# Optimization experiments

Measured on AMD Instinct MI355X. Metric: run time of the kernel, lower is better.

## Reference

```python
import jax, jax.numpy as jnp
import numpy as np

NUM_NODES = 50000
NUM_EDGES = 600000
IN_DIM = 128
HID = 128
OUT_DIM = 10
NUM_GRAPHS = 64


def setup_inputs() -> dict:
    key = jax.random.key(0)
    ks = jax.random.split(key, 12)
    x = jax.random.normal(ks[0], (NUM_NODES, IN_DIM), dtype=jnp.float32)
    edge_index = jax.random.randint(ks[1], (2, NUM_EDGES), 0, NUM_NODES, dtype=jnp.int64)
    batch = jnp.sort(jax.random.randint(ks[2], (NUM_NODES,), 0, NUM_GRAPHS, dtype=jnp.int64))
    s = 0.05
    W1 = jax.random.normal(ks[3], (IN_DIM, HID), dtype=jnp.float32) * s
    b1 = jnp.zeros((HID,), dtype=jnp.float32)
    W2 = jax.random.normal(ks[4], (HID, HID), dtype=jnp.float32) * s
    b2 = jnp.zeros((HID,), dtype=jnp.float32)
    W3 = jax.random.normal(ks[5], (HID, HID), dtype=jnp.float32) * s
    b3 = jnp.zeros((HID,), dtype=jnp.float32)
    Wlin = jax.random.normal(ks[6], (HID, OUT_DIM), dtype=jnp.float32) * s
    blin = jnp.zeros((OUT_DIM,), dtype=jnp.float32)
    return {"x": x, "edge_index": edge_index, "batch": batch,
            "W1": W1, "b1": b1, "W2": W2, "b2": b2, "W3": W3, "b3": b3,
            "Wlin": Wlin, "blin": blin}


def _gcn_conv(x, W, b, src, dst, norm):
    # h = X W ; out[i] = sum_{(j->i)} norm_e * h[j] ; + bias
    h = x @ W                                   # [N, H]
    msg = h[src] * norm[:, None]                # [E+N, H] gather + scale
    out = jax.ops.segment_sum(msg, dst, num_segments=x.shape[0])  # scatter-add
    return out + b


def reference(x, edge_index, batch, W1, b1, W2, b2, W3, b3, Wlin, blin):
    N = x.shape[0]
    # add self loops (PyG GCNConv default)
    loops = jnp.arange(N, dtype=edge_index.dtype)
    src = jnp.concatenate([edge_index[0], loops])
    dst = jnp.concatenate([edge_index[1], loops])
    # symmetric normalization D^{-1/2} (A+I) D^{-1/2}; degree on target nodes
    deg = jax.ops.segment_sum(jnp.ones_like(dst, dtype=x.dtype), dst, num_segments=N)
    dinv = jnp.where(deg > 0, jax.lax.rsqrt(deg), 0.0)
    norm = dinv[src] * dinv[dst]

    h = jax.nn.relu(_gcn_conv(x, W1, b1, src, dst, norm))   # dropout = identity (eval)
    h = jax.nn.relu(_gcn_conv(h, W2, b2, src, dst, norm))
    h = jax.nn.relu(_gcn_conv(h, W3, b3, src, dst, norm))

    # global mean pool over graphs
    sums = jax.ops.segment_sum(h, batch, num_segments=NUM_GRAPHS)          # [G, H]
    cnts = jax.ops.segment_sum(jnp.ones((N,), dtype=h.dtype), batch, num_segments=NUM_GRAPHS)
    pooled = sums / jnp.maximum(cnts, 1.0)[:, None]
    return pooled @ Wlin + blin                                            # [G, OUT]
```

## Files before the change

### kernel.cpp

```cpp
#include <hip/hip_runtime.h>
#include <hip/hip_bf16.h>
#include <hip/hip_fp16.h>


#define HID 128
#define NGRAPH 64

typedef _Float16 half8v __attribute__((ext_vector_type(8)));
typedef float floatx4 __attribute__((ext_vector_type(4)));

__device__ __forceinline__ int idx_at(const void* p, long long i, int f64) {
    if (f64) return (int)((const long long*)p)[i];
    return ((const int*)p)[i];
}

__global__ void detect_kernel(const int* __restrict__ ei, int* __restrict__ flag) {
    __shared__ int cnt;
    if (threadIdx.x == 0) cnt = 0;
    __syncthreads();
    int z = 0;
    for (int i = threadIdx.x; i < 2048; i += 256)
        if (ei[2 * i + 1] == 0) z++;
    atomicAdd(&cnt, z);
    __syncthreads();
    if (threadIdx.x == 0) *flag = (cnt > 1024) ? 1 : 0;
}

__global__ void init_kernel(int* __restrict__ counts, float* __restrict__ pooled,
                            float* __restrict__ gcnt, int N) {
    int i = blockIdx.x * blockDim.x + threadIdx.x;
    if (i < N) counts[i] = 0;
    if (i < NGRAPH * HID) pooled[i] = 0.f;
    if (i < NGRAPH) gcnt[i] = 0.f;
}

__global__ void hist_kernel(const void* __restrict__ ei, const int* __restrict__ flag,
                            int* __restrict__ counts, int E, int N) {
    int e = blockIdx.x * blockDim.x + threadIdx.x;
    if (e >= E) return;
    int f64 = *flag;
    int d = idx_at(ei, (long long)E + e, f64);
    if ((unsigned)d < (unsigned)N) atomicAdd(&counts[d], 1);
}

__global__ __launch_bounds__(256) void tohalf_kernel(const float* __restrict__ in,
                                                     __half2* __restrict__ out, int n2) {
    int i = blockIdx.x * blockDim.x + threadIdx.x;
    if (i >= n2) return;
    float2 v = ((const float2*)in)[i];
    out[i] = __floats2half2_rn(v.x, v.y);
}

__global__ __launch_bounds__(256) void wfrag3_kernel(const float* __restrict__ W1,
                                                     const float* __restrict__ W2,
                                                     const float* __restrict__ W3,
                                                     half8v* __restrict__ wf) {
    int which = blockIdx.x >> 3;
    const float* W = which == 0 ? W1 : (which == 1 ? W2 : W3);
    int t = (blockIdx.x & 7) * 256 + threadIdx.x;
    int lane = t & 63;
    int nt = (t >> 6) & 7;
    int kblk = t >> 9;
    int n = nt * 16 + (lane & 15);
    int kbase = kblk * 32 + (lane >> 4) * 8;
    half8v v;
#pragma unroll
    for (int j = 0; j < 8; ++j) v[j] = (_Float16)W[(size_t)(kbase + j) * 128 + n];
    wf[which * 2048 + t] = v;
}

__device__ __forceinline__ int wave_incl_scan(int v, int lane) {
#pragma unroll
    for (int off = 1; off < 64; off <<= 1) {
        int u = __shfl_up(v, off);
        if (lane >= off) v += u;
    }
    return v;
}

__global__ __launch_bounds__(256) void blocksum_kernel(const int* __restrict__ counts,
                                                       int* __restrict__ bsums, int N) {
    int i = blockIdx.x * 256 + threadIdx.x;
    int v = (i < N) ? counts[i] : 0;
    int lane = threadIdx.x & 63, w = threadIdx.x >> 6;
#pragma unroll
    for (int off = 32; off > 0; off >>= 1) v += __shfl_down(v, off);
    __shared__ int ws[4];
    if (lane == 0) ws[w] = v;
    __syncthreads();
    if (threadIdx.x == 0) bsums[blockIdx.x] = ws[0] + ws[1] + ws[2] + ws[3];
}

__global__ __launch_bounds__(256) void scanb_kernel(int* __restrict__ bsums, int nb) {
    int t = threadIdx.x;
    int lane = t & 63, w = t >> 6;
    int v = (t < nb) ? bsums[t] : 0;
    int iv = wave_incl_scan(v, lane);
    __shared__ int wsum[4];
    if (lane == 63) wsum[w] = iv;
    __syncthreads();
    int add = 0;
    for (int k = 0; k < w; ++k) add += wsum[k];
    if (t < nb) bsums[t] = iv - v + add;
}

__global__ __launch_bounds__(256) void fill_kernel(const int* __restrict__ counts,
                                                   const int* __restrict__ bsums,
                                                   int* __restrict__ rowstart,
                                                   int* __restrict__ cursor,
                                                   float* __restrict__ dinv, int N) {
    int i = blockIdx.x * 256 + threadIdx.x;
    int c = (i < N) ? counts[i] : 0;
    int lane = threadIdx.x & 63, w = threadIdx.x >> 6;
    int iv = wave_incl_scan(c, lane);
    __shared__ int wsum[4];
    if (lane == 63) wsum[w] = iv;
    __syncthreads();
    int add = bsums[blockIdx.x];
    for (int k = 0; k < w; ++k) add += wsum[k];
    int excl = iv - c + add;
    if (i < N) {
        rowstart[i] = excl;
        cursor[i] = excl;
        dinv[i] = rsqrtf((float)(c + 1));
        if (i == N - 1) rowstart[N] = excl + c;
    }
}

__global__ void scatter_kernel(const void* __restrict__ ei, const int* __restrict__ flag,
                               int* __restrict__ cursor,
                               unsigned short* __restrict__ csr_src, int E, int N) {
    int e = blockIdx.x * blockDim.x + threadIdx.x;
    if (e >= E) return;
    int f64 = *flag;
    int s = idx_at(ei, e, f64);
    int d = idx_at(ei, (long long)E + e, f64);
    if ((unsigned)s >= (unsigned)N || (unsigned)d >= (unsigned)N) return;
    int pos = atomicAdd(&cursor[d], 1);
    csr_src[pos] = (unsigned short)s;
}

__global__ __launch_bounds__(256) void agg_kernel(const __half2* __restrict__ xh,
                                                  const int* __restrict__ rowstart,
                                                  const unsigned short* __restrict__ csr_src,
                                                  const float* __restrict__ dinv,
                                                  __half2* __restrict__ out, int N) {
    int wid = (blockIdx.x * blockDim.x + threadIdx.x) >> 6;
    int lane = threadIdx.x & 63;
    if (wid >= N) return;
    float di = dinv[wid];
    float w0 = di * di;
    float2 xs = __half22float2(xh[(size_t)wid * 64 + lane]);
    float accx = w0 * xs.x, accy = w0 * xs.y;
    float bccx = 0.f, bccy = 0.f;
    int e0 = rowstart[wid], e1 = rowstart[wid + 1];
    int e = e0;
    for (; e + 8 <= e1; e += 8) {
        int s[8]; float ds[8]; __half2 v[8];
#pragma unroll
        for (int u = 0; u < 8; ++u) s[u] = csr_src[e + u];
#pragma unroll
        for (int u = 0; u < 8; ++u) ds[u] = dinv[s[u]];
#pragma unroll
        for (int u = 0; u < 8; ++u) v[u] = xh[(size_t)s[u] * 64 + lane];
#pragma unroll
        for (int u = 0; u < 8; u += 2) {
            float wa = ds[u] * di, wb = ds[u + 1] * di;
            float2 f0 = __half22float2(v[u]);
            float2 f1 = __half22float2(v[u + 1]);
            accx = fmaf(wa, f0.x, accx);
            accy = fmaf(wa, f0.y, accy);
            bccx = fmaf(wb, f1.x, bccx);
            bccy = fmaf(wb, f1.y, bccy);
        }
    }
    for (; e + 4 <= e1; e += 4) {
        int s[4]; float ds[4]; __half2 v[4];
#pragma unroll
        for (int u = 0; u < 4; ++u) s[u] = csr_src[e + u];
#pragma unroll
        for (int u = 0; u < 4; ++u) ds[u] = dinv[s[u]];
#pragma unroll
        for (int u = 0; u < 4; ++u) v[u] = xh[(size_t)s[u] * 64 + lane];
#pragma unroll
        for (int u = 0; u < 4; u += 2) {
            float wa = ds[u] * di, wb = ds[u + 1] * di;
            float2 f0 = __half22float2(v[u]);
            float2 f1 = __half22float2(v[u + 1]);
            accx = fmaf(wa, f0.x, accx);
            accy = fmaf(wa, f0.y, accy);
            bccx = fmaf(wb, f1.x, bccx);
            bccy = fmaf(wb, f1.y, bccy);
        }
    }
    for (; e < e1; ++e) {
        int s = csr_src[e];
        float w = dinv[s] * di;
        float2 f = __half22float2(xh[(size_t)s * 64 + lane]);
        accx = fmaf(w, f.x, accx);
        accy = fmaf(w, f.y, accy);
    }
    out[(size_t)wid * 64 + lane] = __floats2half2_rn(accx + bccx, accy + bccy);
}

__global__ __launch_bounds__(256) void gemm_mfma(const __half2* __restrict__ A16,
                                                 const half8v* __restrict__ wf,
                                                 const float* __restrict__ bias,
                                                 __half2* __restrict__ O16, int M) {
    int wid = threadIdx.x >> 6, lane = threadIdx.x & 63;
    int rowTile = blockIdx.x * 64 + wid * 16;
    int hi = lane >> 4;
    int arow = rowTile + (lane & 15);
    if (arow >= M) arow = M - 1;
    const half8v* Arow = (const half8v*)((const _Float16*)A16 + (size_t)arow * 128);

    floatx4 acc[8];
#pragma unroll
    for (int nt = 0; nt < 8; ++nt) acc[nt] = (floatx4){0.f, 0.f, 0.f, 0.f};

#pragma unroll
    for (int kb = 0; kb < 4; ++kb) {
        half8v a = Arow[kb * 4 + hi];
#pragma unroll
        for (int nt = 0; nt < 8; ++nt) {
            half8v w = wf[(kb * 8 + nt) * 64 + lane];
            acc[nt] = __builtin_amdgcn_mfma_f32_16x16x32_f16(a, w, acc[nt], 0, 0, 0);
        }
    }

    int ocol_lo = lane & 15;
    int orow0 = rowTile + hi * 4;
#pragma unroll
    for (int nt = 0; nt < 8; ++nt) {
        int col = nt * 16 + ocol_lo;
        float b = bias[col];
#pragma unroll
        for (int r = 0; r < 4; ++r) {
            int orow = orow0 + r;
            if (orow < M) {
                float v = fmaxf(acc[nt][r] + b, 0.f);
                ((_Float16*)O16)[(size_t)orow * 128 + col] = (_Float16)v;
            }
        }
    }
}

#define POOL_CHUNK 16
__global__ __launch_bounds__(256) void pool_kernel(const __half2* __restrict__ h,
                                                   const void* __restrict__ batch,
                                                   const int* __restrict__ flag,
                                                   float* __restrict__ pooled,
                                                   float* __restrict__ gcnt, int N) {
    int wid = (blockIdx.x * blockDim.x + threadIdx.x) >> 6;
    int lane = threadIdx.x & 63;
    int n0 = wid * POOL_CHUNK;
    if (n0 >= N) return;
    int n1 = n0 + POOL_CHUNK; if (n1 > N) n1 = N;
    int f64 = *flag;
    int g = idx_at(batch, n0, f64);
    float ax = 0.f, ay = 0.f;
    int cnt = 0;
    for (int n = n0; n < n1; ++n) {
        int gn = idx_at(batch, n, f64);
        if (gn != g) {
            if ((unsigned)g < (unsigned)NGRAPH) {
                atomicAdd(&pooled[g * HID + 2 * lane], ax);
                atomicAdd(&pooled[g * HID + 2 * lane + 1], ay);
                if (lane == 0) atomicAdd(&gcnt[g], (float)cnt);
            }
            ax = ay = 0.f; cnt = 0; g = gn;
        }
        float2 v = __half22float2(h[(size_t)n * 64 + lane]);
        ax += v.x; ay += v.y; cnt++;
    }
    if ((unsigned)g < (unsigned)NGRAPH) {
        atomicAdd(&pooled[g * HID + 2 * lane], ax);
        atomicAdd(&pooled[g * HID + 2 * lane + 1], ay);
        if (lane == 0) atomicAdd(&gcnt[g], (float)cnt);
    }
}

__global__ __launch_bounds__(128) void final_kernel(const float* __restrict__ pooled,
                                                    const float* __restrict__ gcnt,
                                                    const float* __restrict__ Wl,
                                                    const float* __restrict__ bl,
                                                    float* __restrict__ out) {
    int o = blockIdx.x * blockDim.x + threadIdx.x;
    if (o >= NGRAPH * 10) return;
    int g = o / 10, c = o % 10;
    float inv = 1.0f / fmaxf(gcnt[g], 1.0f);
    float acc = 0.f;
    for (int k = 0; k < HID; ++k)
        acc = fmaf(pooled[g * HID + k], Wl[k * 10 + c], acc);
    out[o] = acc * inv + bl[c];
}

extern "C" void kernel_launch(void* const* d_in, const int* in_sizes, int n_in,
                              void* d_out, int out_size, void* d_ws, size_t ws_size,
                              hipStream_t stream) {
    const float* x   = (const float*)d_in[0];
    const void* ei   = d_in[1];
    const void* bat  = d_in[2];
    const float* W1  = (const float*)d_in[3];
    const float* b1  = (const float*)d_in[4];
    const float* W2  = (const float*)d_in[5];
    const float* b2  = (const float*)d_in[6];
    const float* W3  = (const float*)d_in[7];
    const float* b3  = (const float*)d_in[8];
    const float* Wl  = (const float*)d_in[9];
    const float* bl  = (const float*)d_in[10];
    float* out = (float*)d_out;

    const int N = in_sizes[0] / HID;
    const int E = in_sizes[1] / 2;

    char* w = (char*)d_ws;
    size_t off = 0;
    auto carve = [&](size_t bytes) -> void* {
        void* p = w + off;
        off = (off + bytes + 255) & ~(size_t)255;
        return p;
    };
    __half2* xh       = (__half2*)carve((size_t)N * HID * 2);
    __half2* aggB16   = (__half2*)carve((size_t)N * HID * 2);
    __half2* h16a     = (__half2*)carve((size_t)N * HID * 2);
    __half2* h16b     = (__half2*)carve((size_t)N * HID * 2);
    int*     counts   = (int*)carve((size_t)N * 4);
    int*     rowstart = (int*)carve((size_t)(N + 1) * 4);
    int*     cursor   = (int*)carve((size_t)N * 4);
    float*   dinv     = (float*)carve((size_t)N * 4);
    unsigned short* csr_src = (unsigned short*)carve((size_t)E * 2);
    float*   pooled   = (float*)carve((size_t)NGRAPH * HID * 4);
    float*   gcnt     = (float*)carve((size_t)NGRAPH * 4);
    half8v*  wf       = (half8v*)carve(3 * 2048 * 16);
    int*     bsums    = (int*)carve(1024);
    int*     flag     = (int*)carve(256);

    const int nb = (N + 255) / 256;

    detect_kernel<<<1, 256, 0, stream>>>((const int*)ei, flag);
    init_kernel<<<(N + 255) / 256, 256, 0, stream>>>(counts, pooled, gcnt, N);
    hist_kernel<<<(E + 255) / 256, 256, 0, stream>>>(ei, flag, counts, E, N);
    blocksum_kernel<<<nb, 256, 0, stream>>>(counts, bsums, N);
    scanb_kernel<<<1, 256, 0, stream>>>(bsums, nb);
    fill_kernel<<<nb, 256, 0, stream>>>(counts, bsums, rowstart, cursor, dinv, N);
    scatter_kernel<<<(E + 255) / 256, 256, 0, stream>>>(ei, flag, cursor, csr_src, E, N);

    const int n2 = N * HID / 2;
    tohalf_kernel<<<(n2 + 255) / 256, 256, 0, stream>>>(x, xh, n2);
    wfrag3_kernel<<<24, 256, 0, stream>>>(W1, W2, W3, wf);

    int aggBlocks  = (N + 3) / 4;
    int gemmBlocks = (N + 63) / 64;

    agg_kernel<<<aggBlocks, 256, 0, stream>>>(xh, rowstart, csr_src, dinv, aggB16, N);
    gemm_mfma<<<gemmBlocks, 256, 0, stream>>>(aggB16, wf, b1, h16a, N);
    agg_kernel<<<aggBlocks, 256, 0, stream>>>(h16a, rowstart, csr_src, dinv, aggB16, N);
    gemm_mfma<<<gemmBlocks, 256, 0, stream>>>(aggB16, wf + 2048, b2, h16b, N);
    agg_kernel<<<aggBlocks, 256, 0, stream>>>(h16b, rowstart, csr_src, dinv, aggB16, N);
    gemm_mfma<<<gemmBlocks, 256, 0, stream>>>(aggB16, wf + 4096, b3, h16a, N);

    int poolWaves = (N + POOL_CHUNK - 1) / POOL_CHUNK;
    int poolBlocks = (poolWaves + 3) / 4;
    pool_kernel<<<poolBlocks, 256, 0, stream>>>(h16a, bat, flag, pooled, gcnt, N);
    final_kernel<<<5, 128, 0, stream>>>(pooled, gcnt, Wl, bl, out);
}
```

Before: 245.2 us.

## Prescale features by dinv to drop per-edge dinv gathers, merge small kernels

Moves the symmetric normalization out of the edge loop. Source features are prescaled by dinv, once in the fp16 conversion and afterwards in the GEMM epilogue, so aggregation becomes a plain sum followed by a single multiply by the destination dinv. This removes one random dinv gather and one multiply per edge in each of the three aggregation passes. The format-detect kernel is folded into init, and the fp16 conversion and weight-fragment kernels are merged into one prep kernel, which cuts launches. Rounding changes slightly because the scaling now happens before the fp16 store.

```diff
diff --git a/kernel.cpp b/kernel.cpp
--- a/kernel.cpp
+++ b/kernel.cpp
@@ -14,24 +14,24 @@
     return ((const int*)p)[i];
 }
 
-__global__ void detect_kernel(const int* __restrict__ ei, int* __restrict__ flag) {
-    __shared__ int cnt;
-    if (threadIdx.x == 0) cnt = 0;
-    __syncthreads();
-    int z = 0;
-    for (int i = threadIdx.x; i < 2048; i += 256)
-        if (ei[2 * i + 1] == 0) z++;
-    atomicAdd(&cnt, z);
-    __syncthreads();
-    if (threadIdx.x == 0) *flag = (cnt > 1024) ? 1 : 0;
-}
-
-__global__ void init_kernel(int* __restrict__ counts, float* __restrict__ pooled,
+__global__ void init_kernel(const int* __restrict__ ei, int* __restrict__ flag,
+                            int* __restrict__ counts, float* __restrict__ pooled,
                             float* __restrict__ gcnt, int N) {
     int i = blockIdx.x * blockDim.x + threadIdx.x;
     if (i < N) counts[i] = 0;
     if (i < NGRAPH * HID) pooled[i] = 0.f;
     if (i < NGRAPH) gcnt[i] = 0.f;
+    if (blockIdx.x == 0) {
+        __shared__ int cnt;
+        if (threadIdx.x == 0) cnt = 0;
+        __syncthreads();
+        int z = 0;
+        for (int k = threadIdx.x; k < 2048; k += 256)
+            if (ei[2 * k + 1] == 0) z++;
+        atomicAdd(&cnt, z);
+        __syncthreads();
+        if (threadIdx.x == 0) *flag = (cnt > 1024) ? 1 : 0;
+    }
 }
 
 __global__ void hist_kernel(const void* __restrict__ ei, const int* __restrict__ flag,
@@ -41,32 +41,6 @@
     int f64 = *flag;
     int d = idx_at(ei, (long long)E + e, f64);
     if ((unsigned)d < (unsigned)N) atomicAdd(&counts[d], 1);
-}
-
-__global__ __launch_bounds__(256) void tohalf_kernel(const float* __restrict__ in,
-                                                     __half2* __restrict__ out, int n2) {
-    int i = blockIdx.x * blockDim.x + threadIdx.x;
-    if (i >= n2) return;
-    float2 v = ((const float2*)in)[i];
-    out[i] = __floats2half2_rn(v.x, v.y);
-}
-
-__global__ __launch_bounds__(256) void wfrag3_kernel(const float* __restrict__ W1,
-                                                     const float* __restrict__ W2,
-                                                     const float* __restrict__ W3,
-                                                     half8v* __restrict__ wf) {
-    int which = blockIdx.x >> 3;
-    const float* W = which == 0 ? W1 : (which == 1 ? W2 : W3);
-    int t = (blockIdx.x & 7) * 256 + threadIdx.x;
-    int lane = t & 63;
-    int nt = (t >> 6) & 7;
-    int kblk = t >> 9;
-    int n = nt * 16 + (lane & 15);
-    int kbase = kblk * 32 + (lane >> 4) * 8;
-    half8v v;
-#pragma unroll
-    for (int j = 0; j < 8; ++j) v[j] = (_Float16)W[(size_t)(kbase + j) * 128 + n];
-    wf[which * 2048 + t] = v;
 }
 
 __device__ __forceinline__ int wave_incl_scan(int v, int lane) {
@@ -140,7 +114,36 @@
     csr_src[pos] = (unsigned short)s;
 }
 
-__global__ __launch_bounds__(256) void agg_kernel(const __half2* __restrict__ xh,
+__global__ __launch_bounds__(256) void prep_kernel(const float* __restrict__ x,
+                                                   const float* __restrict__ dinv,
+                                                   __half2* __restrict__ xs,
+                                                   const float* __restrict__ W1,
+                                                   const float* __restrict__ W2,
+                                                   const float* __restrict__ W3,
+                                                   half8v* __restrict__ wf, int n2) {
+    if (blockIdx.x < 24) {
+        int which = blockIdx.x >> 3;
+        const float* W = which == 0 ? W1 : (which == 1 ? W2 : W3);
+        int t = (blockIdx.x & 7) * 256 + threadIdx.x;
+        int lane = t & 63;
+        int nt = (t >> 6) & 7;
+        int kblk = t >> 9;
+        int n = nt * 16 + (lane & 15);
+        int kbase = kblk * 32 + (lane >> 4) * 8;
+        half8v v;
+#pragma unroll
+        for (int j = 0; j < 8; ++j) v[j] = (_Float16)W[(size_t)(kbase + j) * 128 + n];
+        wf[which * 2048 + t] = v;
+    } else {
+        int i = (blockIdx.x - 24) * 256 + threadIdx.x;
+        if (i >= n2) return;
+        float dv = dinv[i >> 6];
+        float2 v = ((const float2*)x)[i];
+        xs[i] = __floats2half2_rn(dv * v.x, dv * v.y);
+    }
+}
+
+__global__ __launch_bounds__(256) void agg_kernel(const __half2* __restrict__ xs,
                                                   const int* __restrict__ rowstart,
                                                   const unsigned short* __restrict__ csr_src,
                                                   const float* __restrict__ dinv,
@@ -149,63 +152,53 @@
     int lane = threadIdx.x & 63;
     if (wid >= N) return;
     float di = dinv[wid];
-    float w0 = di * di;
-    float2 xs = __half22float2(xh[(size_t)wid * 64 + lane]);
-    float accx = w0 * xs.x, accy = w0 * xs.y;
+    float2 s0 = __half22float2(xs[(size_t)wid * 64 + lane]);
+    float accx = s0.x, accy = s0.y;
     float bccx = 0.f, bccy = 0.f;
     int e0 = rowstart[wid], e1 = rowstart[wid + 1];
     int e = e0;
     for (; e + 8 <= e1; e += 8) {
-        int s[8]; float ds[8]; __half2 v[8];
+        int s[8]; __half2 v[8];
 #pragma unroll
         for (int u = 0; u < 8; ++u) s[u] = csr_src[e + u];
 #pragma unroll
-        for (int u = 0; u < 8; ++u) ds[u] = dinv[s[u]];
-#pragma unroll
-        for (int u = 0; u < 8; ++u) v[u] = xh[(size_t)s[u] * 64 + lane];
+        for (int u = 0; u < 8; ++u) v[u] = xs[(size_t)s[u] * 64 + lane];
 #pragma unroll
         for (int u = 0; u < 8; u += 2) {
-            float wa = ds[u] * di, wb = ds[u + 1] * di;
             float2 f0 = __half22float2(v[u]);
             float2 f1 = __half22float2(v[u + 1]);
-            accx = fmaf(wa, f0.x, accx);
-            accy = fmaf(wa, f0.y, accy);
-            bccx = fmaf(wb, f1.x, bccx);
-            bccy = fmaf(wb, f1.y, bccy);
+            accx += f0.x; accy += f0.y;
+            bccx += f1.x; bccy += f1.y;
         }
     }
     for (; e + 4 <= e1; e += 4) {
-        int s[4]; float ds[4]; __half2 v[4];
+        int s[4]; __half2 v[4];
 #pragma unroll
         for (int u = 0; u < 4; ++u) s[u] = csr_src[e + u];
 #pragma unroll
-        for (int u = 0; u < 4; ++u) ds[u] = dinv[s[u]];
-#pragma unroll
-        for (int u = 0; u < 4; ++u) v[u] = xh[(size_t)s[u] * 64 + lane];
+        for (int u = 0; u < 4; ++u) v[u] = xs[(size_t)s[u] * 64 + lane];
 #pragma unroll
         for (int u = 0; u < 4; u += 2) {
-            float wa = ds[u] * di, wb = ds[u + 1] * di;
             float2 f0 = __half22float2(v[u]);
             float2 f1 = __half22float2(v[u + 1]);
-            accx = fmaf(wa, f0.x, accx);
-            accy = fmaf(wa, f0.y, accy);
-            bccx = fmaf(wb, f1.x, bccx);
-            bccy = fmaf(wb, f1.y, bccy);
+            accx += f0.x; accy += f0.y;
+            bccx += f1.x; bccy += f1.y;
         }
     }
     for (; e < e1; ++e) {
         int s = csr_src[e];
-        float w = dinv[s] * di;
-        float2 f = __half22float2(xh[(size_t)s * 64 + lane]);
-        accx = fmaf(w, f.x, accx);
-        accy = fmaf(w, f.y, accy);
-    }
-    out[(size_t)wid * 64 + lane] = __floats2half2_rn(accx + bccx, accy + bccy);
-}
-
+        float2 f = __half22float2(xs[(size_t)s * 64 + lane]);
+        accx += f.x; accy += f.y;
+    }
+    out[(size_t)wid * 64 + lane] = __floats2half2_rn(di * (accx + bccx),
+                                                     di * (accy + bccy));
+}
+
+template <bool SCALED>
 __global__ __launch_bounds__(256) void gemm_mfma(const __half2* __restrict__ A16,
                                                  const half8v* __restrict__ wf,
                                                  const float* __restrict__ bias,
+                                                 const float* __restrict__ dinv,
                                                  __half2* __restrict__ O16, int M) {
     int wid = threadIdx.x >> 6, lane = threadIdx.x & 63;
     int rowTile = blockIdx.x * 64 + wid * 16;
@@ -230,6 +223,12 @@
 
     int ocol_lo = lane & 15;
     int orow0 = rowTile + hi * 4;
+    float dv[4];
+#pragma unroll
+    for (int r = 0; r < 4; ++r) {
+        int orow = orow0 + r;
+        dv[r] = (SCALED && orow < M) ? dinv[orow] : 1.0f;
+    }
 #pragma unroll
     for (int nt = 0; nt < 8; ++nt) {
         int col = nt * 16 + ocol_lo;
@@ -239,6 +238,7 @@
             int orow = orow0 + r;
             if (orow < M) {
                 float v = fmaxf(acc[nt][r] + b, 0.f);
+                if (SCALED) v *= dv[r];
                 ((_Float16*)O16)[(size_t)orow * 128 + col] = (_Float16)v;
             }
         }
@@ -321,10 +321,10 @@
         off = (off + bytes + 255) & ~(size_t)255;
         return p;
     };
-    __half2* xh       = (__half2*)carve((size_t)N * HID * 2);
+    __half2* xs       = (__half2*)carve((size_t)N * HID * 2);
     __half2* aggB16   = (__half2*)carve((size_t)N * HID * 2);
-    __half2* h16a     = (__half2*)carve((size_t)N * HID * 2);
-    __half2* h16b     = (__half2*)carve((size_t)N * HID * 2);
+    __half2* hsA      = (__half2*)carve((size_t)N * HID * 2);
+    __half2* hsB      = (__half2*)carve((size_t)N * HID * 2);
     int*     counts   = (int*)carve((size_t)N * 4);
     int*     rowstart = (int*)carve((size_t)(N + 1) * 4);
     int*     cursor   = (int*)carve((size_t)N * 4);
@@ -337,31 +337,29 @@
     int*     flag     = (int*)carve(256);
 
     const int nb = (N + 255) / 256;
-
-    detect_kernel<<<1, 256, 0, stream>>>((const int*)ei, flag);
-    init_kernel<<<(N + 255) / 256, 256, 0, stream>>>(counts, pooled, gcnt, N);
+    const int n2 = N * HID / 2;
+
+    init_kernel<<<nb, 256, 0, stream>>>((const int*)ei, flag, counts, pooled, gcnt, N);
     hist_kernel<<<(E + 255) / 256, 256, 0, stream>>>(ei, flag, counts, E, N);
     blocksum_kernel<<<nb, 256, 0, stream>>>(counts, bsums, N);
     scanb_kernel<<<1, 256, 0, stream>>>(bsums, nb);
     fill_kernel<<<nb, 256, 0, stream>>>(counts, bsums, rowstart, cursor, dinv, N);
     scatter_kernel<<<(E + 255) / 256, 256, 0, stream>>>(ei, flag, cursor, csr_src, E, N);
-
-    const int n2 = N * HID / 2;
-    tohalf_kernel<<<(n2 + 255) / 256, 256, 0, stream>>>(x, xh, n2);
-    wfrag3_kernel<<<24, 256, 0, stream>>>(W1, W2, W3, wf);
+    prep_kernel<<<24 + (n2 + 255) / 256, 256, 0, stream>>>(x, dinv, xs,
+                                                           W1, W2, W3, wf, n2);
 
     int aggBlocks  = (N + 3) / 4;
     int gemmBlocks = (N + 63) / 64;
 
-    agg_kernel<<<aggBlocks, 256, 0, stream>>>(xh, rowstart, csr_src, dinv, aggB16, N);
-    gemm_mfma<<<gemmBlocks, 256, 0, stream>>>(aggB16, wf, b1, h16a, N);
-    agg_kernel<<<aggBlocks, 256, 0, stream>>>(h16a, rowstart, csr_src, dinv, aggB16, N);
-    gemm_mfma<<<gemmBlocks, 256, 0, stream>>>(aggB16, wf + 2048, b2, h16b, N);
-    agg_kernel<<<aggBlocks, 256, 0, stream>>>(h16b, rowstart, csr_src, dinv, aggB16, N);
-    gemm_mfma<<<gemmBlocks, 256, 0, stream>>>(aggB16, wf + 4096, b3, h16a, N);
+    agg_kernel<<<aggBlocks, 256, 0, stream>>>(xs, rowstart, csr_src, dinv, aggB16, N);
+    gemm_mfma<true><<<gemmBlocks, 256, 0, stream>>>(aggB16, wf, b1, dinv, hsA, N);
+    agg_kernel<<<aggBlocks, 256, 0, stream>>>(hsA, rowstart, csr_src, dinv, aggB16, N);
+    gemm_mfma<true><<<gemmBlocks, 256, 0, stream>>>(aggB16, wf + 2048, b2, dinv, hsB, N);
+    agg_kernel<<<aggBlocks, 256, 0, stream>>>(hsB, rowstart, csr_src, dinv, aggB16, N);
+    gemm_mfma<false><<<gemmBlocks, 256, 0, stream>>>(aggB16, wf + 4096, b3, dinv, hsA, N);
 
     int poolWaves = (N + POOL_CHUNK - 1) / POOL_CHUNK;
     int poolBlocks = (poolWaves + 3) / 4;
-    pool_kernel<<<poolBlocks, 256, 0, stream>>>(h16a, bat, flag, pooled, gcnt, N);
+    pool_kernel<<<poolBlocks, 256, 0, stream>>>(hsA, bat, flag, pooled, gcnt, N);
     final_kernel<<<5, 128, 0, stream>>>(pooled, gcnt, Wl, bl, out);
 }
```

After: 240.9 us. Within noise of the previous version (-1.7%).
